# Performance work log

Measured on AMD Instinct MI355X. Metric: run time of the kernel, lower is better.

## Reference

```python
import jax, jax.numpy as jnp
import numpy as np

SCALING = 16.0 / 16.0  # lora_alpha / r

def setup_inputs() -> dict:
    key = jax.random.key(0)
    k1, k2, k3, k4, k5 = jax.random.split(key, 5)
    B, S, D, R = 4, 4096, 4096, 16
    x = jax.random.normal(k1, (B, S, D), dtype=jnp.float32)
    W = jax.random.normal(k2, (D, D), dtype=jnp.float32) * (1.0 / np.sqrt(D))
    bias = jax.random.normal(k3, (D,), dtype=jnp.float32) * 0.02
    lora_A = jax.random.normal(k4, (D, R), dtype=jnp.float32) * (1.0 / np.sqrt(D))
    lora_B = jax.random.normal(k5, (R, D), dtype=jnp.float32) * 0.02
    return {"x": x, "W": W, "bias": bias, "lora_A": lora_A, "lora_B": lora_B}

def reference(x, W, bias, lora_A, lora_B):
    x_dtype = x.dtype
    # base (quantized) linear modeled as dense GEMM: [B,S,D] @ [D,D]
    out = jnp.einsum('bsd,df->bsf', x, W)
    # low-rank LoRA path: (x @ A) @ B * scaling, computed in train_dtype then cast back
    lora = jnp.einsum('bsr,rf->bsf', jnp.einsum('bsd,dr->bsr', x.astype(lora_A.dtype), lora_A), lora_B) * SCALING
    out = out + lora.astype(x_dtype)
    out = out + bias.astype(x_dtype)
    return out
```

## Files before the change

### kernel.cpp

```cpp
#include <hip/hip_runtime.h>
#include <hip/hip_bf16.h>


typedef __attribute__((ext_vector_type(8))) __bf16 bf16x8;
typedef __attribute__((ext_vector_type(4))) float f32x4;

#define M_DIM 16384
#define N_DIM 4096
#define K_DIM 4096

__device__ __forceinline__ void async16(const void* g, void* l) {
    __builtin_amdgcn_global_load_lds((const __attribute__((address_space(1))) void*)g,
                                     (__attribute__((address_space(3))) void*)l,
                                     16, 0, 0);
}

__global__ void cast_x_kernel(const float* __restrict__ x, __bf16* __restrict__ xb, size_t n) {
    size_t i0 = ((size_t)blockIdx.x * blockDim.x + threadIdx.x) * 8;
    size_t stride = (size_t)gridDim.x * blockDim.x * 8;
    for (size_t i = i0; i < n; i += stride) {
        f32x4 v0 = __builtin_nontemporal_load((const f32x4*)(x + i));
        f32x4 v1 = __builtin_nontemporal_load((const f32x4*)(x + i + 4));
        bf16x8 o;
        o[0] = (__bf16)v0[0]; o[1] = (__bf16)v0[1]; o[2] = (__bf16)v0[2]; o[3] = (__bf16)v0[3];
        o[4] = (__bf16)v1[0]; o[5] = (__bf16)v1[1]; o[6] = (__bf16)v1[2]; o[7] = (__bf16)v1[3];
        *(bf16x8*)(xb + i) = o;
    }
}

__global__ void prep_w_kernel(const float* __restrict__ W, const float* __restrict__ A,
                              const float* __restrict__ Bm, __bf16* __restrict__ Wt) {
    __shared__ float Ws[32][33];
    __shared__ float As[32][16];
    __shared__ float Bs[16][32];
    const int tx = threadIdx.x;
    const int ty = threadIdx.y;
    const int t = ty * 32 + tx;
    const int n0 = blockIdx.x * 32;
    const int k0 = blockIdx.y * 32;

#pragma unroll
    for (int i = 0; i < 4; ++i) {
        int k = ty + i * 8;
        Ws[k][tx] = W[(size_t)(k0 + k) * N_DIM + n0 + tx];
    }
    for (int i = t; i < 512; i += 256)
        As[i >> 4][i & 15] = A[(size_t)(k0 + (i >> 4)) * 16 + (i & 15)];
    for (int i = t; i < 512; i += 256)
        Bs[i >> 5][i & 31] = Bm[(size_t)(i >> 5) * N_DIM + n0 + (i & 31)];
    __syncthreads();

    float a[16];
#pragma unroll
    for (int r = 0; r < 16; ++r) a[r] = As[tx][r];
#pragma unroll
    for (int i = 0; i < 4; ++i) {
        int n = ty + i * 8;
        float acc = Ws[tx][n];
#pragma unroll
        for (int r = 0; r < 16; ++r) acc += a[r] * Bs[r][n];
        Wt[(size_t)(n0 + n) * K_DIM + k0 + tx] = (__bf16)acc;
    }
}


#define WAIT_VM(N) asm volatile("s_waitcnt vmcnt(" #N ")" ::: "memory")
#define BARRIER() do { asm volatile("" ::: "memory"); __builtin_amdgcn_s_barrier(); asm volatile("" ::: "memory"); } while (0)

#define ST(ptr, koff, ldsbase, row0) \
    async16((ptr) + (koff), (ldsbase) + (row0) * 128 + sldsoff)

#define LOAD_AF(dst, ldsbase, MH)                                                    \
    _Pragma("unroll") for (int m_ = 0; m_ < 4; ++m_)                                 \
    _Pragma("unroll") for (int ks_ = 0; ks_ < 2; ++ks_)                              \
        dst[m_][ks_] = *(const bf16x8*)((ldsbase) + aRowB + (MH) * 8192 + m_ * 2048 + colsw[ks_]);

#define LOAD_BF(dst, ldsbase, NH)                                                    \
    _Pragma("unroll") for (int n_ = 0; n_ < 2; ++n_)                                 \
    _Pragma("unroll") for (int ks_ = 0; ks_ < 2; ++ks_)                              \
        dst[n_][ks_] = *(const bf16x8*)((ldsbase) + bRowB + (NH) * 16384 + n_ * 2048 + colsw[ks_]);

#define MFMA_Q(AF, MB, NB, BF)                                                       \
    __builtin_amdgcn_s_setprio(1);                                                   \
    _Pragma("unroll") for (int m_ = 0; m_ < 4; ++m_)                                 \
    _Pragma("unroll") for (int n_ = 0; n_ < 2; ++n_)                                 \
    _Pragma("unroll") for (int ks_ = 0; ks_ < 2; ++ks_)                              \
        acc[(MB) + m_][(NB) + n_] = __builtin_amdgcn_mfma_f32_16x16x32_bf16(         \
            AF[m_][ks_], BF[n_][ks_], acc[(MB) + m_][(NB) + n_], 0, 0, 0);           \
    __builtin_amdgcn_s_setprio(0);

#define TILE_FULL(AC, BC, AO, BO, KT)                                                \
    LOAD_AF(afr0, AC, 0); LOAD_BF(b0f, BC, 0);                                       \
    ST(pB0, (KT) + 64, BO, 0);    ST(pB1, (KT) + 64, BO, 64);                        \
    ST(pA1, (KT) + 64, AO, 64);   ST(pA3, (KT) + 64, AO, 192);                       \
    BARRIER(); MFMA_Q(afr0, 0, 0, b0f);                                              \
    LOAD_BF(b1f, BC, 1);                                                             \
    BARRIER(); MFMA_Q(afr0, 0, 2, b1f);                                              \
    LOAD_AF(afr1, AC, 1);                                                            \
    ST(pA0, (KT) + 128, AC, 0);   ST(pA2, (KT) + 128, AC, 128);                      \
    BARRIER(); MFMA_Q(afr1, 4, 2, b1f);                                              \
    ST(pB2, (KT) + 128, BC, 128); ST(pB3, (KT) + 128, BC, 192);                      \
    WAIT_VM(4);                                                                      \
    BARRIER(); MFMA_Q(afr1, 4, 0, b0f);

__global__ __launch_bounds__(512, 2) void gemm256_kernel(
    const __bf16* __restrict__ Xb, const __bf16* __restrict__ Wt,
    const float* __restrict__ bias, float* __restrict__ out) {
    extern __shared__ __align__(16) char smem[];
    const int tid  = threadIdx.x;
    const int lane = tid & 63;
    const int wave = tid >> 6;
    const int wr = wave >> 2;
    const int wn = wave & 3;

    const int bid = blockIdx.x;
    const int wg = (bid & 7) * 128 + (bid >> 3);
    const int m0 = (wg >> 4) * 256;
    const int n0 = (wg & 15) * 256;

    char* A0 = smem;
    char* B0 = smem + 32768;
    char* A1 = smem + 65536;
    char* B1 = smem + 98304;

    const int srow = tid >> 3;
    const int scol = ((tid & 7) ^ (srow & 7)) << 3;
    const int sldsoff = wave * 1024;

    const __bf16* pA0 = Xb + (size_t)(m0 + 0   + srow) * K_DIM + scol;
    const __bf16* pA1 = Xb + (size_t)(m0 + 64  + srow) * K_DIM + scol;
    const __bf16* pA2 = Xb + (size_t)(m0 + 128 + srow) * K_DIM + scol;
    const __bf16* pA3 = Xb + (size_t)(m0 + 192 + srow) * K_DIM + scol;
#define BPERM(P) ((((P) >> 5) & 3) * 64 + (((P) >> 7) & 1) * 32 + ((P) & 31))
    const __bf16* pB0 = Wt + (size_t)(n0 + BPERM(0   + srow)) * K_DIM + scol;
    const __bf16* pB1 = Wt + (size_t)(n0 + BPERM(64  + srow)) * K_DIM + scol;
    const __bf16* pB2 = Wt + (size_t)(n0 + BPERM(128 + srow)) * K_DIM + scol;
    const __bf16* pB3 = Wt + (size_t)(n0 + BPERM(192 + srow)) * K_DIM + scol;

    int colsw[2];
#pragma unroll
    for (int ks = 0; ks < 2; ++ks)
        colsw[ks] = ((ks * 32 + (lane >> 4) * 8) ^ ((lane & 7) * 8)) << 1;
    const int aRowB = (wr * 128 + (lane & 15)) * 128;
    const int bRowB = (wn * 32 + (lane & 15)) * 128;

    f32x4 acc[8][4] = {};
    bf16x8 afr0[4][2], afr1[4][2], b0f[2][2], b1f[2][2];

    ST(pA0, 0, A0, 0);    ST(pA2, 0, A0, 128);
    ST(pA1, 0, A0, 64);   ST(pA3, 0, A0, 192);
    ST(pB0, 0, B0, 0);    ST(pB1, 0, B0, 64);
    ST(pB2, 0, B0, 128);  ST(pB3, 0, B0, 192);
    ST(pA0, 64, A1, 0);   ST(pA2, 64, A1, 128);
    ST(pB2, 64, B1, 128); ST(pB3, 64, B1, 192);
    WAIT_VM(4);
    BARRIER();

    for (int it = 0; it < 31; ++it) {
        const int kt = it * 128;
        TILE_FULL(A0, B0, A1, B1, kt);
        TILE_FULL(A1, B1, A0, B0, kt + 64);
    }

    LOAD_AF(afr0, A0, 0); LOAD_BF(b0f, B0, 0);
    ST(pB0, 4032, B1, 0);  ST(pB1, 4032, B1, 64);
    ST(pA1, 4032, A1, 64); ST(pA3, 4032, A1, 192);
    BARRIER(); MFMA_Q(afr0, 0, 0, b0f);
    LOAD_BF(b1f, B0, 1);
    BARRIER(); MFMA_Q(afr0, 0, 2, b1f);
    LOAD_AF(afr1, A0, 1);
    BARRIER(); MFMA_Q(afr1, 4, 2, b1f);
    WAIT_VM(0);
    BARRIER(); MFMA_Q(afr1, 4, 0, b0f);

    LOAD_AF(afr0, A1, 0); LOAD_BF(b0f, B1, 0);
    LOAD_BF(b1f, B1, 1);  LOAD_AF(afr1, A1, 1);
    MFMA_Q(afr0, 0, 0, b0f);
    MFMA_Q(afr0, 0, 2, b1f);
    MFMA_Q(afr1, 4, 2, b1f);
    MFMA_Q(afr1, 4, 0, b0f);

    float* cbuf = (float*)smem;
#pragma unroll
    for (int mh = 0; mh < 2; ++mh) {
        BARRIER();
#pragma unroll
        for (int m = 0; m < 4; ++m)
#pragma unroll
            for (int nh = 0; nh < 2; ++nh)
#pragma unroll
                for (int n = 0; n < 2; ++n) {
                    const int lc = wn * 64 + nh * 32 + n * 16 + (lane & 15);
                    const float bv = bias[n0 + lc];
                    const f32x4 a = acc[mh * 4 + m][nh * 2 + n];
#pragma unroll
                    for (int j = 0; j < 4; ++j) {
                        const int r = wr * 64 + m * 16 + (lane >> 4) * 4 + j;
                        cbuf[r * 256 + ((lc + 4 * r) & 255)] = a[j] + bv;
                    }
                }
        BARRIER();
#pragma unroll
        for (int i = 0; i < 16; ++i) {
            const int idx = i * 512 + tid;
            const int r = idx >> 6;
            const int c4 = idx & 63;
            const f32x4 v = *(const f32x4*)&cbuf[r * 256 + (((c4 + r) & 63) << 2)];
            const int grow = m0 + mh * 64 + r + ((r >> 6) << 6);
            __builtin_nontemporal_store(v,
                (f32x4*)&out[(size_t)grow * N_DIM + n0 + c4 * 4]);
        }
    }
}

extern "C" void kernel_launch(void* const* d_in, const int* in_sizes, int n_in,
                              void* d_out, int out_size, void* d_ws, size_t ws_size,
                              hipStream_t stream) {
    const float* x    = (const float*)d_in[0];
    const float* W    = (const float*)d_in[1];
    const float* bias = (const float*)d_in[2];
    const float* lA   = (const float*)d_in[3];
    const float* lB   = (const float*)d_in[4];
    float* out = (float*)d_out;

    __bf16* Xb = (__bf16*)d_ws;
    __bf16* Wt = (__bf16*)((char*)d_ws + (size_t)M_DIM * K_DIM * 2);

    cast_x_kernel<<<2048, 256, 0, stream>>>(x, Xb, (size_t)M_DIM * K_DIM);
    prep_w_kernel<<<dim3(N_DIM / 32, K_DIM / 32), dim3(32, 8), 0, stream>>>(W, lA, lB, Wt);

    (void)hipFuncSetAttribute((const void*)gemm256_kernel,
                              hipFuncAttributeMaxDynamicSharedMemorySize, 131072);
    gemm256_kernel<<<1024, 512, 131072, stream>>>(Xb, Wt, bias, out);
}
```

Baseline: 540.9 us.

## Restructure GEMM main loop to two barriers per K-tile with prefetched fragments

Result: slower. 931.4 us (+72.2%).

```diff
diff --git a/kernel.cpp b/kernel.cpp
--- a/kernel.cpp
+++ b/kernel.cpp
@@ -89,19 +89,18 @@
             AF[m_][ks_], BF[n_][ks_], acc[(MB) + m_][(NB) + n_], 0, 0, 0);           \
     __builtin_amdgcn_s_setprio(0);
 
-#define TILE_FULL(AC, BC, AO, BO, KT)                                                \
-    LOAD_AF(afr0, AC, 0); LOAD_BF(b0f, BC, 0);                                       \
-    ST(pB0, (KT) + 64, BO, 0);    ST(pB1, (KT) + 64, BO, 64);                        \
-    ST(pA1, (KT) + 64, AO, 64);   ST(pA3, (KT) + 64, AO, 192);                       \
-    BARRIER(); MFMA_Q(afr0, 0, 0, b0f);                                              \
-    LOAD_BF(b1f, BC, 1);                                                             \
-    BARRIER(); MFMA_Q(afr0, 0, 2, b1f);                                              \
+#define TILE_2B(AC, BC, AO, BO, KT)                                                  \
+    MFMA_Q(afr0, 0, 0, b0f); MFMA_Q(afr0, 0, 2, b1f);                                \
     LOAD_AF(afr1, AC, 1);                                                            \
-    ST(pA0, (KT) + 128, AC, 0);   ST(pA2, (KT) + 128, AC, 128);                      \
-    BARRIER(); MFMA_Q(afr1, 4, 2, b1f);                                              \
+    ST(pB0, (KT) + 128, BC, 0);   ST(pB1, (KT) + 128, BC, 64);                       \
     ST(pB2, (KT) + 128, BC, 128); ST(pB3, (KT) + 128, BC, 192);                      \
     WAIT_VM(4);                                                                      \
-    BARRIER(); MFMA_Q(afr1, 4, 0, b0f);
+    BARRIER();                                                                       \
+    MFMA_Q(afr1, 4, 2, b1f); MFMA_Q(afr1, 4, 0, b0f);                                \
+    LOAD_AF(afr0, AO, 0); LOAD_BF(b0f, BO, 0); LOAD_BF(b1f, BO, 1);                  \
+    ST(pA0, (KT) + 128, AC, 0);   ST(pA2, (KT) + 128, AC, 128);                      \
+    ST(pA1, (KT) + 128, AC, 64);  ST(pA3, (KT) + 128, AC, 192);                      \
+    BARRIER();
 
 __global__ __launch_bounds__(512, 2) void gemm256_kernel(
     const __bf16* __restrict__ Xb, const __bf16* __restrict__ Wt,
@@ -147,38 +146,36 @@
     f32x4 acc[8][4] = {};
     bf16x8 afr0[4][2], afr1[4][2], b0f[2][2], b1f[2][2];
 
-    ST(pA0, 0, A0, 0);    ST(pA2, 0, A0, 128);
-    ST(pA1, 0, A0, 64);   ST(pA3, 0, A0, 192);
-    ST(pB0, 0, B0, 0);    ST(pB1, 0, B0, 64);
-    ST(pB2, 0, B0, 128);  ST(pB3, 0, B0, 192);
-    ST(pA0, 64, A1, 0);   ST(pA2, 64, A1, 128);
+    ST(pA0, 0, A0, 0);   ST(pA2, 0, A0, 128);
+    ST(pA1, 0, A0, 64);  ST(pA3, 0, A0, 192);
+    ST(pB0, 0, B0, 0);   ST(pB1, 0, B0, 64);
+    ST(pB2, 0, B0, 128); ST(pB3, 0, B0, 192);
+    ST(pB0, 64, B1, 0);  ST(pB1, 64, B1, 64);
     ST(pB2, 64, B1, 128); ST(pB3, 64, B1, 192);
     WAIT_VM(4);
     BARRIER();
+    LOAD_AF(afr0, A0, 0); LOAD_BF(b0f, B0, 0); LOAD_BF(b1f, B0, 1);
+    ST(pA0, 64, A1, 0);  ST(pA2, 64, A1, 128);
+    ST(pA1, 64, A1, 64); ST(pA3, 64, A1, 192);
+    BARRIER();
 
     for (int it = 0; it < 31; ++it) {
         const int kt = it * 128;
-        TILE_FULL(A0, B0, A1, B1, kt);
-        TILE_FULL(A1, B1, A0, B0, kt + 64);
-    }
-
-    LOAD_AF(afr0, A0, 0); LOAD_BF(b0f, B0, 0);
-    ST(pB0, 4032, B1, 0);  ST(pB1, 4032, B1, 64);
-    ST(pA1, 4032, A1, 64); ST(pA3, 4032, A1, 192);
-    BARRIER(); MFMA_Q(afr0, 0, 0, b0f);
-    LOAD_BF(b1f, B0, 1);
-    BARRIER(); MFMA_Q(afr0, 0, 2, b1f);
+        TILE_2B(A0, B0, A1, B1, kt);
+        TILE_2B(A1, B1, A0, B0, kt + 64);
+    }
+
+    MFMA_Q(afr0, 0, 0, b0f); MFMA_Q(afr0, 0, 2, b1f);
     LOAD_AF(afr1, A0, 1);
-    BARRIER(); MFMA_Q(afr1, 4, 2, b1f);
     WAIT_VM(0);
-    BARRIER(); MFMA_Q(afr1, 4, 0, b0f);
-
-    LOAD_AF(afr0, A1, 0); LOAD_BF(b0f, B1, 0);
-    LOAD_BF(b1f, B1, 1);  LOAD_AF(afr1, A1, 1);
-    MFMA_Q(afr0, 0, 0, b0f);
-    MFMA_Q(afr0, 0, 2, b1f);
-    MFMA_Q(afr1, 4, 2, b1f);
-    MFMA_Q(afr1, 4, 0, b0f);
+    BARRIER();
+    MFMA_Q(afr1, 4, 2, b1f); MFMA_Q(afr1, 4, 0, b0f);
+    LOAD_AF(afr0, A1, 0); LOAD_BF(b0f, B1, 0); LOAD_BF(b1f, B1, 1);
+    BARRIER();
+
+    MFMA_Q(afr0, 0, 0, b0f); MFMA_Q(afr0, 0, 2, b1f);
+    LOAD_AF(afr1, A1, 1);
+    MFMA_Q(afr1, 4, 2, b1f); MFMA_Q(afr1, 4, 0, b0f);
 
     float* cbuf = (float*)smem;
 #pragma unroll
```
